# Kernel tuning notes

Hardware: AMD Instinct MI355X
Metric: run time of the kernel (lower is better)

## Reference

```python
import jax, jax.numpy as jnp
import numpy as np

B = 16384
NUM_RATE, NUM_GENRE, NUM_DIRECTOR, NUM_ACTOR = 6, 25, 2186, 8030
EMB = 32


def setup_inputs() -> dict:
    key = jax.random.key(0)
    k0, k1, k2, k3, k4 = jax.random.split(key, 5)
    x = jax.random.randint(k0, (B, 1 + NUM_GENRE + NUM_DIRECTOR + NUM_ACTOR), 0, 2, dtype=jnp.int64 if jax.config.jax_enable_x64 else jnp.int32)
    rate_table = jax.random.normal(k1, (NUM_RATE, EMB), dtype=jnp.float32)
    # torch Linear weights have shape [out_features, in_features]
    W_genre = jax.random.normal(k2, (EMB, NUM_GENRE), dtype=jnp.float32) * (1.0 / np.sqrt(NUM_GENRE))
    W_director = jax.random.normal(k3, (EMB, NUM_DIRECTOR), dtype=jnp.float32) * (1.0 / np.sqrt(NUM_DIRECTOR))
    W_actor = jax.random.normal(k4, (EMB, NUM_ACTOR), dtype=jnp.float32) * (1.0 / np.sqrt(NUM_ACTOR))
    return {"x": x, "rate_table": rate_table, "W_genre": W_genre,
            "W_director": W_director, "W_actor": W_actor}


def _maxnorm_gather(table, idx, max_norm=1.0, eps=1e-7):
    # torch.nn.Embedding(max_norm=1.0): rows accessed are renormalized to norm <= max_norm
    rows = table[idx]  # [B, E]
    norm = jnp.linalg.norm(rows, axis=-1, keepdims=True)
    scale = jnp.where(norm > max_norm, max_norm / (norm + eps), 1.0)
    return rows * scale


def _mean_pool_linear(multi_hot_f, W):
    # Linear(no bias) on multi-hot then divide by row-sum == mean-pooled embedding bag
    emb = jnp.einsum('bn,en->be', multi_hot_f, W)
    return emb / jnp.sum(multi_hot_f, axis=1, keepdims=True)


def reference(x, rate_table, W_genre, W_director, W_actor):
    rate_idx = x[:, 0]
    genre = x[:, 1:26].astype(jnp.float32)
    director = x[:, 26:2212].astype(jnp.float32)
    actors = x[:, 2212:10242].astype(jnp.float32)
    rate_emb = _maxnorm_gather(rate_table, rate_idx)
    genre_emb = _mean_pool_linear(genre, W_genre)
    director_emb = _mean_pool_linear(director, W_director)
    actors_emb = _mean_pool_linear(actors, W_actor)
    return jnp.concatenate((rate_emb, genre_emb, director_emb, actors_emb), axis=1)  # [B, 4*EMB]
```

## Files before the change

### kernel.cpp

```cpp
#include <hip/hip_runtime.h>
#include <hip/hip_bf16.h>

#define B_ROWS 16384
#define XC     10242
#define NGENRE 25
#define NDIR   2186
#define NACT   8030
#define EMB    32
#define KT_TOTAL 321
#define OUTC   128
#define NCOLS  112
#define PART_STRIDE ((size_t)B_ROWS * NCOLS)
#define WFRAG_BYTES ((size_t)KT_TOTAL * 4 * 64 * 16)

typedef short bf16x8 __attribute__((ext_vector_type(8)));
typedef float f32x4  __attribute__((ext_vector_type(4)));
typedef float f32x4a __attribute__((ext_vector_type(4), aligned(4)));
typedef int   i32x4a __attribute__((ext_vector_type(4), aligned(4)));

__global__ void prep_wfrag(const float* __restrict__ wg,
                           const float* __restrict__ wd,
                           const float* __restrict__ wa,
                           uint4* __restrict__ Wfrag) {
  const int kt = blockIdx.x;
  const int s  = threadIdx.x >> 6;
  const int l  = threadIdx.x & 63;
  const int n  = l & 15;
  const int k0 = kt * 32 + ((l >> 4) << 3);

  float f[8];
  bool done = false;
  if (s < 2) {
    if (kt >= 1 && kt < 69) {
      const float* p = wd + (size_t)(s * 16 + n) * NDIR + (k0 - 26);
      f32x4a v0 = *reinterpret_cast<const f32x4a*>(p);
      f32x4a v1 = *reinterpret_cast<const f32x4a*>(p + 4);
      f[0]=v0[0]; f[1]=v0[1]; f[2]=v0[2]; f[3]=v0[3];
      f[4]=v1[0]; f[5]=v1[1]; f[6]=v1[2]; f[7]=v1[3];
      done = true;
    } else if (kt >= 70 && kt < 320) {
      const float* p = wa + (size_t)(s * 16 + n) * NACT + (k0 - 2212);
      f32x4a v0 = *reinterpret_cast<const f32x4a*>(p);
      f32x4a v1 = *reinterpret_cast<const f32x4a*>(p + 4);
      f[0]=v0[0]; f[1]=v0[1]; f[2]=v0[2]; f[3]=v0[3];
      f[4]=v1[0]; f[5]=v1[1]; f[6]=v1[2]; f[7]=v1[3];
      done = true;
    }
  }
  if (!done) {
#pragma unroll
    for (int j = 0; j < 8; ++j) {
      const int k = k0 + j;
      float v = 0.f;
      if (kt == 0) {
        if (s < 2) { if (k >= 1 && k < 26) v = wg[(s * 16 + n) * NGENRE + (k - 1)]; }
        else       { if (k >= 26)          v = wd[((s - 2) * 16 + n) * NDIR + (k - 26)]; }
      } else if (kt == 69) {
        if (s < 2) { if (k < 2212)  v = wd[(s * 16 + n) * NDIR + (k - 26)]; }
        else       { if (k >= 2212) v = wa[((s - 2) * 16 + n) * NACT + (k - 2212)]; }
      } else if (kt == 320) {
        if (s < 2 && k < XC) v = wa[(s * 16 + n) * NACT + (k - 2212)];
      }
      f[j] = v;
    }
  }
  union { unsigned short u[8]; uint4 q; } cv;
#pragma unroll
  for (int j = 0; j < 8; ++j) {
    __hip_bfloat16 h = __float2bfloat16(f[j]);
    cv.u[j] = *reinterpret_cast<unsigned short*>(&h);
  }
  Wfrag[((size_t)kt * 4 + s) * 64 + l] = cv.q;
}

template<int KS>
__global__ __launch_bounds__(256) void main_mm(const int* __restrict__ x,
                                               const uint4* __restrict__ Wfrag,
                                               float* __restrict__ part) {
  constexpr int PER = (((KT_TOTAL + KS - 1) / KS) + 3) & ~3;
  const int t    = threadIdx.x;
  const int rb   = blockIdx.x & 255;
  const int ks   = blockIdx.x >> 8;
  const int ktA  = ks * PER;
  const int ktB  = (ktA + PER < KT_TOTAL) ? ktA + PER : KT_TOTAL;
  const int lane = t & 63;
  const int w    = t >> 6;
  const int lo   = lane & 15, hi = lane >> 4;
  const int* xrow = x + (size_t)(rb * 64 + w * 16 + lo) * XC;

  f32x4 accG0 = {0,0,0,0}, accG1 = {0,0,0,0};
  f32x4 accD0 = {0,0,0,0}, accD1 = {0,0,0,0};
  f32x4 accA0 = {0,0,0,0}, accA1 = {0,0,0,0};
  f32x4 accI  = {0,0,0,0};

  auto load_x8 = [&](int kt, int* dst) {
    int k0 = kt * 32 + hi * 8;
    if (kt < 320) {
      i32x4a a = *reinterpret_cast<const i32x4a*>(xrow + k0);
      i32x4a b = *reinterpret_cast<const i32x4a*>(xrow + k0 + 4);
      dst[0]=a[0]; dst[1]=a[1]; dst[2]=a[2]; dst[3]=a[3];
      dst[4]=b[0]; dst[5]=b[1]; dst[6]=b[2]; dst[7]=b[3];
    } else {
#pragma unroll
      for (int j = 0; j < 8; ++j) dst[j] = (k0 + j < XC) ? xrow[k0 + j] : 0;
    }
  };
  auto packa = [&](const int* cx) -> bf16x8 {
    union { unsigned int w4[4]; bf16x8 v; } af;
#pragma unroll
    for (int i = 0; i < 4; ++i)
      af.w4[i] = ((unsigned)cx[2*i] + ((unsigned)cx[2*i+1] << 16)) * 0x3F80u;
    return af.v;
  };
  auto bload = [&](int kt, int s) -> bf16x8 {
    union { uint4 q; bf16x8 v; } c;
    c.q = Wfrag[((size_t)kt * 4 + s) * 64 + lane];
    return c.v;
  };
  auto mkconst = [&](bool on) -> bf16x8 {
    union { unsigned int w4[4]; bf16x8 v; } c;
    unsigned int u = on ? 0x3F803F80u : 0u;
    c.w4[0]=u; c.w4[1]=u; c.w4[2]=u; c.w4[3]=u;
    return c.v;
  };
  const bf16x8 ivD = mkconst(lo == 1);
  const bf16x8 ivA = mkconst(lo == 2);

  auto do_mfma = [&](int kt, bf16x8 a, bf16x8 b0, bf16x8 b1) {
    const int kb = kt * 32 + hi * 8;
    if (kt == 0) {
      accG0 = __builtin_amdgcn_mfma_f32_16x16x32_bf16(a, b0, accG0, 0,0,0);
      accG1 = __builtin_amdgcn_mfma_f32_16x16x32_bf16(a, b1, accG1, 0,0,0);
      accD0 = __builtin_amdgcn_mfma_f32_16x16x32_bf16(a, bload(0,2), accD0, 0,0,0);
      accD1 = __builtin_amdgcn_mfma_f32_16x16x32_bf16(a, bload(0,3), accD1, 0,0,0);
      union { unsigned short u[8]; bf16x8 v; } iv;
#pragma unroll
      for (int j = 0; j < 8; ++j) {
        int k = kb + j;
        bool on = (lo == 0) ? (k >= 1 && k < 26) : (lo == 1) ? (k >= 26) : false;
        iv.u[j] = on ? (unsigned short)0x3F80 : (unsigned short)0;
      }
      accI = __builtin_amdgcn_mfma_f32_16x16x32_bf16(a, iv.v, accI, 0,0,0);
    } else if (kt < 69) {
      accD0 = __builtin_amdgcn_mfma_f32_16x16x32_bf16(a, b0, accD0, 0,0,0);
      accD1 = __builtin_amdgcn_mfma_f32_16x16x32_bf16(a, b1, accD1, 0,0,0);
      accI  = __builtin_amdgcn_mfma_f32_16x16x32_bf16(a, ivD, accI, 0,0,0);
    } else if (kt == 69) {
      accD0 = __builtin_amdgcn_mfma_f32_16x16x32_bf16(a, b0, accD0, 0,0,0);
      accD1 = __builtin_amdgcn_mfma_f32_16x16x32_bf16(a, b1, accD1, 0,0,0);
      accA0 = __builtin_amdgcn_mfma_f32_16x16x32_bf16(a, bload(69,2), accA0, 0,0,0);
      accA1 = __builtin_amdgcn_mfma_f32_16x16x32_bf16(a, bload(69,3), accA1, 0,0,0);
      union { unsigned short u[8]; bf16x8 v; } iv;
#pragma unroll
      for (int j = 0; j < 8; ++j) {
        int k = kb + j;
        bool on = (lo == 1) ? (k < 2212) : (lo == 2) ? (k >= 2212) : false;
        iv.u[j] = on ? (unsigned short)0x3F80 : (unsigned short)0;
      }
      accI = __builtin_amdgcn_mfma_f32_16x16x32_bf16(a, iv.v, accI, 0,0,0);
    } else if (kt < 320) {
      accA0 = __builtin_amdgcn_mfma_f32_16x16x32_bf16(a, b0, accA0, 0,0,0);
      accA1 = __builtin_amdgcn_mfma_f32_16x16x32_bf16(a, b1, accA1, 0,0,0);
      accI  = __builtin_amdgcn_mfma_f32_16x16x32_bf16(a, ivA, accI, 0,0,0);
    } else {
      accA0 = __builtin_amdgcn_mfma_f32_16x16x32_bf16(a, b0, accA0, 0,0,0);
      accA1 = __builtin_amdgcn_mfma_f32_16x16x32_bf16(a, b1, accA1, 0,0,0);
      union { unsigned short u[8]; bf16x8 v; } iv;
#pragma unroll
      for (int j = 0; j < 8; ++j) {
        int k = kb + j;
        iv.u[j] = (lo == 2 && k < XC) ? (unsigned short)0x3F80 : (unsigned short)0;
      }
      accI = __builtin_amdgcn_mfma_f32_16x16x32_bf16(a, iv.v, accI, 0,0,0);
    }
  };

  int xA0[8], xA1[8], xA2[8], xA3[8];
  int xB0[8], xB1[8], xB2[8], xB3[8];

  auto load_group = [&](int g, int* d0, int* d1, int* d2, int* d3) {
    if (g     < ktB) load_x8(g,     d0);
    if (g + 1 < ktB) load_x8(g + 1, d1);
    if (g + 2 < ktB) load_x8(g + 2, d2);
    if (g + 3 < ktB) load_x8(g + 3, d3);
  };

  auto run_group = [&](int g,
                       const int* s0, const int* s1, const int* s2, const int* s3,
                       int* d0, int* d1, int* d2, int* d3) {
    bf16x8 b00 = bload(g, 0), b01 = bload(g, 1);
    bf16x8 b10, b11, b20, b21, b30, b31;
    if (g + 1 < ktB) { b10 = bload(g + 1, 0); b11 = bload(g + 1, 1); }
    if (g + 2 < ktB) { b20 = bload(g + 2, 0); b21 = bload(g + 2, 1); }
    if (g + 3 < ktB) { b30 = bload(g + 3, 0); b31 = bload(g + 3, 1); }
    load_group(g + 4, d0, d1, d2, d3);
    do_mfma(g, packa(s0), b00, b01);
    if (g + 1 < ktB) do_mfma(g + 1, packa(s1), b10, b11);
    if (g + 2 < ktB) do_mfma(g + 2, packa(s2), b20, b21);
    if (g + 3 < ktB) do_mfma(g + 3, packa(s3), b30, b31);
  };

  load_group(ktA, xA0, xA1, xA2, xA3);
  for (int g = ktA; g < ktB; g += 8) {
    run_group(g,     xA0, xA1, xA2, xA3, xB0, xB1, xB2, xB3);
    if (g + 4 < ktB)
      run_group(g + 4, xB0, xB1, xB2, xB3, xA0, xA1, xA2, xA3);
  }

  float* slab = part + (size_t)ks * PART_STRIDE;
  const int rbase = rb * 64 + w * 16 + hi * 4;
#pragma unroll
  for (int j = 0; j < 4; ++j) {
    size_t ro = (size_t)(rbase + j) * NCOLS;
    slab[ro +  0 + lo] = accG0[j];
    slab[ro + 16 + lo] = accG1[j];
    slab[ro + 32 + lo] = accD0[j];
    slab[ro + 48 + lo] = accD1[j];
    slab[ro + 64 + lo] = accA0[j];
    slab[ro + 80 + lo] = accA1[j];
    if (lo < 3) slab[ro + 96 + lo] = accI[j];
  }
}

__global__ __launch_bounds__(128) void reduce_k(const int* __restrict__ x,
                                                const float* __restrict__ rate,
                                                const float* __restrict__ part,
                                                int ksplit,
                                                float* __restrict__ out) {
  __shared__ float srow[112];
  const int r = blockIdx.x;
  const int c = threadIdx.x;

  if (c < 28) {
    f32x4 acc = {0.f, 0.f, 0.f, 0.f};
    for (int ks = 0; ks < ksplit; ++ks) {
      const float* p = part + (size_t)ks * PART_STRIDE + (size_t)r * NCOLS + c * 4;
      f32x4a v = *reinterpret_cast<const f32x4a*>(p);
      acc[0] += v[0]; acc[1] += v[1]; acc[2] += v[2]; acc[3] += v[3];
    }
    srow[c * 4 + 0] = acc[0];
    srow[c * 4 + 1] = acc[1];
    srow[c * 4 + 2] = acc[2];
    srow[c * 4 + 3] = acc[3];
  }
  __syncthreads();

  float res;
  if (c < EMB) {
    int idx = x[(size_t)r * XC];
    float v = rate[idx * EMB + c];
    float s2 = v * v;
    s2 += __shfl_xor(s2, 1, 32);
    s2 += __shfl_xor(s2, 2, 32);
    s2 += __shfl_xor(s2, 4, 32);
    s2 += __shfl_xor(s2, 8, 32);
    s2 += __shfl_xor(s2, 16, 32);
    float norm = sqrtf(s2);
    float scale = (norm > 1.0f) ? (1.0f / (norm + 1e-7f)) : 1.0f;
    res = v * scale;
  } else {
    int cc = c - EMB;
    res = srow[cc] / srow[96 + (cc >> 5)];
  }
  out[(size_t)r * OUTC + c] = res;
}

extern "C" void kernel_launch(void* const* d_in, const int* in_sizes, int n_in,
                              void* d_out, int out_size, void* d_ws, size_t ws_size,
                              hipStream_t stream) {
  (void)in_sizes; (void)n_in; (void)out_size;
  const int*   x    = (const int*)d_in[0];
  const float* rate = (const float*)d_in[1];
  const float* wg   = (const float*)d_in[2];
  const float* wd   = (const float*)d_in[3];
  const float* wa   = (const float*)d_in[4];
  float* out  = (float*)d_out;
  float* part = (float*)d_ws;

  const size_t slab_bytes = PART_STRIDE * sizeof(float);
  int KS;
  if      (ws_size >= 4 * slab_bytes + WFRAG_BYTES) KS = 4;
  else if (ws_size >= 2 * slab_bytes + WFRAG_BYTES) KS = 2;
  else                                              KS = 1;
  uint4* Wfrag = (uint4*)((char*)d_ws + (size_t)KS * slab_bytes);

  prep_wfrag<<<KT_TOTAL, 256, 0, stream>>>(wg, wd, wa, Wfrag);
  switch (KS) {
    case 4: main_mm<4><<<4 * 256, 256, 0, stream>>>(x, Wfrag, part); break;
    case 2: main_mm<2><<<2 * 256, 256, 0, stream>>>(x, Wfrag, part); break;
    default: main_mm<1><<<1 * 256, 256, 0, stream>>>(x, Wfrag, part); break;
  }
  reduce_k<<<B_ROWS, 128, 0, stream>>>(x, rate, part, KS, out);
}
```

Baseline: 899.6 us.

## Pre-pack multi-hot input into bitmasks before the MFMA pass

Adds a pack_x kernel that compresses each 32-column tile of the int32 multi-hot input into one 32-bit mask, stored with a padded row stride. The main MFMA kernel then loads four mask words per group and expands them into bf16 A-fragments in registers, instead of streaming the full int32 rows. The goal is to separate the bandwidth-heavy read of x from the compute pass and to simplify the software pipelining of B-fragment and mask loads. The cost is an extra full read of x plus a kernel launch, and more workspace.

Result: no change. 913.3 us (+1.5%).

```diff
diff --git a/kernel.cpp b/kernel.cpp
--- a/kernel.cpp
+++ b/kernel.cpp
@@ -8,15 +8,40 @@
 #define NACT   8030
 #define EMB    32
 #define KT_TOTAL 321
+#define XB_STRIDE 328
 #define OUTC   128
 #define NCOLS  112
 #define PART_STRIDE ((size_t)B_ROWS * NCOLS)
 #define WFRAG_BYTES ((size_t)KT_TOTAL * 4 * 64 * 16)
+#define XB_BYTES    ((size_t)B_ROWS * XB_STRIDE * 4)
 
 typedef short bf16x8 __attribute__((ext_vector_type(8)));
 typedef float f32x4  __attribute__((ext_vector_type(4)));
 typedef float f32x4a __attribute__((ext_vector_type(4), aligned(4)));
 typedef int   i32x4a __attribute__((ext_vector_type(4), aligned(4)));
+
+__global__ __launch_bounds__(256) void pack_x(const int* __restrict__ x,
+                                              unsigned* __restrict__ xb) {
+  const int w0 = blockIdx.x * 256 + threadIdx.x;
+  if (w0 >= B_ROWS * KT_TOTAL) return;
+  const int r  = w0 / KT_TOTAL;
+  const int kt = w0 - r * KT_TOTAL;
+  const int* p = x + (size_t)r * XC + kt * 32;
+  unsigned m = 0;
+  if (kt < 320) {
+#pragma unroll
+    for (int i = 0; i < 8; ++i) {
+      i32x4a v = *reinterpret_cast<const i32x4a*>(p + 4 * i);
+      m |= ((unsigned)(v[0] & 1) << (4 * i))
+         | ((unsigned)(v[1] & 1) << (4 * i + 1))
+         | ((unsigned)(v[2] & 1) << (4 * i + 2))
+         | ((unsigned)(v[3] & 1) << (4 * i + 3));
+    }
+  } else {
+    m = (unsigned)(p[0] & 1) | ((unsigned)(p[1] & 1) << 1);
+  }
+  xb[(size_t)r * XB_STRIDE + kt] = m;
+}
 
 __global__ void prep_wfrag(const float* __restrict__ wg,
                            const float* __restrict__ wd,
@@ -73,8 +98,10 @@
   Wfrag[((size_t)kt * 4 + s) * 64 + l] = cv.q;
 }
 
+struct BSet { bf16x8 b00, b01, b10, b11, b20, b21, b30, b31; };
+
 template<int KS>
-__global__ __launch_bounds__(256) void main_mm(const int* __restrict__ x,
+__global__ __launch_bounds__(256) void main_mm(const unsigned* __restrict__ xb,
                                                const uint4* __restrict__ Wfrag,
                                                float* __restrict__ part) {
   constexpr int PER = (((KT_TOTAL + KS - 1) / KS) + 3) & ~3;
@@ -86,36 +113,30 @@
   const int lane = t & 63;
   const int w    = t >> 6;
   const int lo   = lane & 15, hi = lane >> 4;
-  const int* xrow = x + (size_t)(rb * 64 + w * 16 + lo) * XC;
+  const unsigned* xbrow = xb + (size_t)(rb * 64 + w * 16 + lo) * XB_STRIDE;
 
   f32x4 accG0 = {0,0,0,0}, accG1 = {0,0,0,0};
   f32x4 accD0 = {0,0,0,0}, accD1 = {0,0,0,0};
   f32x4 accA0 = {0,0,0,0}, accA1 = {0,0,0,0};
   f32x4 accI  = {0,0,0,0};
 
-  auto load_x8 = [&](int kt, int* dst) {
-    int k0 = kt * 32 + hi * 8;
-    if (kt < 320) {
-      i32x4a a = *reinterpret_cast<const i32x4a*>(xrow + k0);
-      i32x4a b = *reinterpret_cast<const i32x4a*>(xrow + k0 + 4);
-      dst[0]=a[0]; dst[1]=a[1]; dst[2]=a[2]; dst[3]=a[3];
-      dst[4]=b[0]; dst[5]=b[1]; dst[6]=b[2]; dst[7]=b[3];
-    } else {
-#pragma unroll
-      for (int j = 0; j < 8; ++j) dst[j] = (k0 + j < XC) ? xrow[k0 + j] : 0;
-    }
-  };
-  auto packa = [&](const int* cx) -> bf16x8 {
-    union { unsigned int w4[4]; bf16x8 v; } af;
-#pragma unroll
-    for (int i = 0; i < 4; ++i)
-      af.w4[i] = ((unsigned)cx[2*i] + ((unsigned)cx[2*i+1] << 16)) * 0x3F80u;
-    return af.v;
-  };
   auto bload = [&](int kt, int s) -> bf16x8 {
     union { uint4 q; bf16x8 v; } c;
     c.q = Wfrag[((size_t)kt * 4 + s) * 64 + lane];
     return c.v;
+  };
+  auto ldm = [&](int g) -> i32x4a {
+    return *reinterpret_cast<const i32x4a*>(xbrow + g);
+  };
+  auto afrag = [&](int mi) -> bf16x8 {
+    const unsigned m = (unsigned)mi;
+    union { unsigned w4[4]; bf16x8 v; } af;
+#pragma unroll
+    for (int i = 0; i < 4; ++i) {
+      unsigned tt = m >> (hi * 8 + 2 * i);
+      af.w4[i] = ((tt & 1u) * 0x3F80u) + (((tt >> 1) & 1u) * 0x3F800000u);
+    }
+    return af.v;
   };
   auto mkconst = [&](bool on) -> bf16x8 {
     union { unsigned int w4[4]; bf16x8 v; } c;
@@ -175,36 +196,34 @@
     }
   };
 
-  int xA0[8], xA1[8], xA2[8], xA3[8];
-  int xB0[8], xB1[8], xB2[8], xB3[8];
-
-  auto load_group = [&](int g, int* d0, int* d1, int* d2, int* d3) {
-    if (g     < ktB) load_x8(g,     d0);
-    if (g + 1 < ktB) load_x8(g + 1, d1);
-    if (g + 2 < ktB) load_x8(g + 2, d2);
-    if (g + 3 < ktB) load_x8(g + 3, d3);
-  };
-
-  auto run_group = [&](int g,
-                       const int* s0, const int* s1, const int* s2, const int* s3,
-                       int* d0, int* d1, int* d2, int* d3) {
-    bf16x8 b00 = bload(g, 0), b01 = bload(g, 1);
-    bf16x8 b10, b11, b20, b21, b30, b31;
-    if (g + 1 < ktB) { b10 = bload(g + 1, 0); b11 = bload(g + 1, 1); }
-    if (g + 2 < ktB) { b20 = bload(g + 2, 0); b21 = bload(g + 2, 1); }
-    if (g + 3 < ktB) { b30 = bload(g + 3, 0); b31 = bload(g + 3, 1); }
-    load_group(g + 4, d0, d1, d2, d3);
-    do_mfma(g, packa(s0), b00, b01);
-    if (g + 1 < ktB) do_mfma(g + 1, packa(s1), b10, b11);
-    if (g + 2 < ktB) do_mfma(g + 2, packa(s2), b20, b21);
-    if (g + 3 < ktB) do_mfma(g + 3, packa(s3), b30, b31);
-  };
-
-  load_group(ktA, xA0, xA1, xA2, xA3);
+  auto bload4 = [&](int g) -> BSet {
+    BSet s;
+    s.b00 = bload(g, 0); s.b01 = bload(g, 1);
+    if (g + 1 < ktB) { s.b10 = bload(g + 1, 0); s.b11 = bload(g + 1, 1); }
+    if (g + 2 < ktB) { s.b20 = bload(g + 2, 0); s.b21 = bload(g + 2, 1); }
+    if (g + 3 < ktB) { s.b30 = bload(g + 3, 0); s.b31 = bload(g + 3, 1); }
+    return s;
+  };
+  auto consume = [&](int g, const BSet& s, i32x4a mm) {
+    do_mfma(g, afrag(mm[0]), s.b00, s.b01);
+    if (g + 1 < ktB) do_mfma(g + 1, afrag(mm[1]), s.b10, s.b11);
+    if (g + 2 < ktB) do_mfma(g + 2, afrag(mm[2]), s.b20, s.b21);
+    if (g + 3 < ktB) do_mfma(g + 3, afrag(mm[3]), s.b30, s.b31);
+  };
+
+  BSet sE, sO;
+  i32x4a mE = {0,0,0,0}, mO = {0,0,0,0};
+  sE = bload4(ktA);
+  mE = ldm(ktA);
+  if (ktA + 4 < ktB) { sO = bload4(ktA + 4); mO = ldm(ktA + 4); }
+
   for (int g = ktA; g < ktB; g += 8) {
-    run_group(g,     xA0, xA1, xA2, xA3, xB0, xB1, xB2, xB3);
-    if (g + 4 < ktB)
-      run_group(g + 4, xB0, xB1, xB2, xB3, xA0, xA1, xA2, xA3);
+    consume(g, sE, mE);
+    if (g + 8 < ktB) { sE = bload4(g + 8); mE = ldm(g + 8); }
+    if (g + 4 < ktB) {
+      consume(g + 4, sO, mO);
+      if (g + 12 < ktB) { sO = bload4(g + 12); mO = ldm(g + 12); }
+    }
   }
 
   float* slab = part + (size_t)ks * PART_STRIDE;
@@ -279,16 +298,19 @@
 
   const size_t slab_bytes = PART_STRIDE * sizeof(float);
   int KS;
-  if      (ws_size >= 4 * slab_bytes + WFRAG_BYTES) KS = 4;
-  else if (ws_size >= 2 * slab_bytes + WFRAG_BYTES) KS = 2;
-  else                                              KS = 1;
-  uint4* Wfrag = (uint4*)((char*)d_ws + (size_t)KS * slab_bytes);
-
+  if      (ws_size >= 4 * slab_bytes + WFRAG_BYTES + XB_BYTES) KS = 4;
+  else if (ws_size >= 2 * slab_bytes + WFRAG_BYTES + XB_BYTES) KS = 2;
+  else                                                         KS = 1;
+  uint4*    Wfrag = (uint4*)((char*)d_ws + (size_t)KS * slab_bytes);
+  unsigned* xbp   = (unsigned*)((char*)d_ws + (size_t)KS * slab_bytes + WFRAG_BYTES);
+
+  const int nwords = B_ROWS * KT_TOTAL;
+  pack_x<<<(nwords + 255) / 256, 256, 0, stream>>>(x, xbp);
   prep_wfrag<<<KT_TOTAL, 256, 0, stream>>>(wg, wd, wa, Wfrag);
   switch (KS) {
-    case 4: main_mm<4><<<4 * 256, 256, 0, stream>>>(x, Wfrag, part); break;
-    case 2: main_mm<2><<<2 * 256, 256, 0, stream>>>(x, Wfrag, part); break;
-    default: main_mm<1><<<1 * 256, 256, 0, stream>>>(x, Wfrag, part); break;
+    case 4: main_mm<4><<<4 * 256, 256, 0, stream>>>(xbp, Wfrag, part); break;
+    case 2: main_mm<2><<<2 * 256, 256, 0, stream>>>(xbp, Wfrag, part); break;
+    default: main_mm<1><<<1 * 256, 256, 0, stream>>>(xbp, Wfrag, part); break;
   }
   reduce_k<<<B_ROWS, 128, 0, stream>>>(x, rate, part, KS, out);
 }
```
